# Kernel optimization log

Hardware: AMD Instinct MI355X
Metric: run time of the kernel (lower is better)

The kernel has to match this reference:

```python
import jax, jax.numpy as jnp
import numpy as np

B, S, E, H, FF = 4, 2048, 512, 8, 2048
DH = E // H
EPS = 1e-6


def setup_inputs() -> dict:
    key = jax.random.key(0)
    ks = jax.random.split(key, 16)
    sc = lambda fan_in: 1.0 / np.sqrt(fan_in)
    inp = {
        "x": jax.random.normal(ks[0], (B, S, E), dtype=jnp.float32),
        "src_mask": jnp.ones((B, 1, 1, S), dtype=jnp.int32),
        # attention projections, stored [in, out]
        "wq": jax.random.uniform(ks[1], (E, E), minval=-sc(E), maxval=sc(E)),
        "bq": jnp.zeros((E,), jnp.float32),
        "wk": jax.random.uniform(ks[2], (E, E), minval=-sc(E), maxval=sc(E)),
        "bk": jnp.zeros((E,), jnp.float32),
        "wv": jax.random.uniform(ks[3], (E, E), minval=-sc(E), maxval=sc(E)),
        "bv": jnp.zeros((E,), jnp.float32),
        "wo": jax.random.uniform(ks[4], (E, E), minval=-sc(E), maxval=sc(E)),
        "bo": jnp.zeros((E,), jnp.float32),
        # feed-forward
        "w1": jax.random.uniform(ks[5], (E, FF), minval=-sc(E), maxval=sc(E)),
        "b1": jnp.zeros((FF,), jnp.float32),
        "w2": jax.random.uniform(ks[6], (FF, E), minval=-sc(FF), maxval=sc(FF)),
        "b2": jnp.zeros((E,), jnp.float32),
        # addNormLayer scalar params (alpha init 1, bias init 0)
        "alpha1": jnp.ones((1,), jnp.float32),
        "beta1": jnp.zeros((1,), jnp.float32),
        "alpha2": jnp.ones((1,), jnp.float32),
        "beta2": jnp.zeros((1,), jnp.float32),
    }
    return inp


def _norm(x, alpha, beta):
    # matches torch: mean + unbiased std (ddof=1), eps added to std
    mean = jnp.mean(x, axis=-1, keepdims=True)
    std = jnp.std(x, axis=-1, keepdims=True, ddof=1)
    return alpha * (x - mean) / (std + EPS) + beta


def reference(x, src_mask, wq, bq, wk, bk, wv, bv, wo, bo,
              w1, b1, w2, b2, alpha1, beta1, alpha2, beta2):
    # --- residual 1: pre-norm self-attention ---
    n = _norm(x, alpha1, beta1)  # [B,S,E]
    q = (n @ wq + bq).reshape(B, S, H, DH).transpose(0, 2, 1, 3)  # [B,H,S,DH]
    k = (n @ wk + bk).reshape(B, S, H, DH).transpose(0, 2, 1, 3)
    v = (n @ wv + bv).reshape(B, S, H, DH).transpose(0, 2, 1, 3)
    scores = jnp.einsum('bhqd,bhkd->bhqk', q, k) / np.sqrt(DH)  # [B,H,S,S]
    scores = jnp.where(src_mask == 0, -1e9, scores)
    attn = jax.nn.softmax(scores, axis=-1)
    ctx = jnp.einsum('bhqk,bhkd->bhqd', attn, v)  # [B,H,S,DH]
    ctx = ctx.transpose(0, 2, 1, 3).reshape(B, S, E)
    x = x + (ctx @ wo + bo)
    # --- residual 2: pre-norm FFN ---
    n2 = _norm(x, alpha2, beta2)
    ff = jax.nn.relu(n2 @ w1 + b1) @ w2 + b2
    return x + ff
```

## Files before the change

### kernel.cpp

```cpp
#include <hip/hip_runtime.h>

typedef __bf16 bfrag __attribute__((ext_vector_type(8)));
typedef float f32x4 __attribute__((ext_vector_type(4)));
typedef float f32x16 __attribute__((ext_vector_type(16)));
typedef unsigned short us8 __attribute__((ext_vector_type(8)));
typedef unsigned int u32x2 __attribute__((ext_vector_type(2)));
typedef unsigned int u32x4 __attribute__((ext_vector_type(4)));

__device__ __forceinline__ float bf2f(unsigned short s) {
  unsigned u = ((unsigned)s) << 16;
  float f;
  __builtin_memcpy(&f, &u, 4);
  return f;
}
__device__ __forceinline__ unsigned short f2bf(float f) {
  unsigned u;
  __builtin_memcpy(&u, &f, 4);
  u += 0x7fffu + ((u >> 16) & 1u);
  return (unsigned short)(u >> 16);
}
__device__ __forceinline__ float rdf(const void* p, size_t i, int isf) {
  return isf ? ((const float*)p)[i] : bf2f(((const unsigned short*)p)[i]);
}
__device__ __forceinline__ void gld16(const unsigned short* g, unsigned short* l) {
  __builtin_amdgcn_global_load_lds(
      (const __attribute__((address_space(1))) unsigned int*)g,
      (__attribute__((address_space(3))) unsigned int*)l, 16, 0, 0);
}
__device__ __forceinline__ unsigned cvtpk_bf16(float a, float b) {
  unsigned d;
  asm("v_cvt_pk_bf16_f32 %0, %1, %2" : "=v"(d) : "v"(a), "v"(b));
  return d;
}

template <int XMODE>
__device__ void norm_unit(const void* xin, const void* alpha, const void* beta,
                          unsigned short* out, int isf, int u) {
  constexpr int E = 512;
  int xf = XMODE ? 1 : isf;
  int tid = threadIdx.x;
  int wave = tid >> 6, lane = tid & 63;
  size_t tok = (size_t)u * 4 + wave;
  float v[8];
  if (xf) {
    const float* xp = (const float*)xin + tok * E + lane * 8;
    float4 a0 = *(const float4*)xp;
    float4 a1 = *(const float4*)(xp + 4);
    v[0] = a0.x; v[1] = a0.y; v[2] = a0.z; v[3] = a0.w;
    v[4] = a1.x; v[5] = a1.y; v[6] = a1.z; v[7] = a1.w;
  } else {
    us8 uu = *(const us8*)((const unsigned short*)xin + tok * E + lane * 8);
#pragma unroll
    for (int j = 0; j < 8; j++) v[j] = bf2f(uu[j]);
  }
  float s = 0.f, sq = 0.f;
#pragma unroll
  for (int j = 0; j < 8; j++) { s += v[j]; sq += v[j] * v[j]; }
#pragma unroll
  for (int off = 1; off < 64; off <<= 1) {
    s += __shfl_xor(s, off, 64);
    sq += __shfl_xor(sq, off, 64);
  }
  float mean = s * (1.0f / 512.0f);
  float var = fmaxf((sq - 512.0f * mean * mean) * (1.0f / 511.0f), 0.0f);
  float inv = rdf(alpha, 0, isf) / (sqrtf(var) + 1e-6f);
  float be = rdf(beta, 0, isf);
  us8 ov;
#pragma unroll
  for (int j = 0; j < 8; j++) ov[j] = f2bf((v[j] - mean) * inv + be);
  *(us8*)(out + tok * E + lane * 8) = ov;
}

__global__ __launch_bounds__(256) void setup_k(
    const unsigned short* __restrict__ x16,
    const void* wq, const void* wk, const void* wv, const void* wo,
    const void* w1, const void* w2,
    unsigned short* wqkvT, unsigned short* woT,
    unsigned short* w1T, unsigned short* w2T,
    const void* bq, const void* bk, const void* bv, const void* bo,
    const void* b1, const void* b2, float* __restrict__ bcat,
    const void* alpha1, const void* beta1, unsigned short* __restrict__ n1,
    int* __restrict__ flag) {
  __shared__ unsigned short tile[32][33];
  __shared__ int s_cnt;
  int tid = threadIdx.x;
  int bid = blockIdx.x;
  if (tid == 0) s_cnt = 0;
  __syncthreads();
  {
    int c = 0;
    for (int i = tid; i < 4096; i += 256) {
      unsigned short s = x16[2 * i];
      int e = (s >> 7) & 0xFF;
      if (e > 0xC2 || (e != 0 && e < 0x3D)) c++;
    }
    atomicAdd(&s_cnt, c);
  }
  __syncthreads();
  const int isf = (s_cnt > 256) ? 1 : 0;
  if (bid == 0 && tid == 0) flag[0] = isf;

  if (bid >= 3090) {
    norm_unit<0>(x16, alpha1, beta1, n1, isf, bid - 3090);
    return;
  }
  if (bid >= 3072) {
    int i = (bid - 3072) * 256 + tid;
    if (i < 4608) {
      float v;
      if (i < 512) v = rdf(bq, i, isf);
      else if (i < 1024) v = rdf(bk, i - 512, isf);
      else if (i < 1536) v = rdf(bv, i - 1024, isf);
      else if (i < 2048) v = rdf(bo, i - 1536, isf);
      else if (i < 4096) v = rdf(b1, i - 2048, isf);
      else v = rdf(b2, i - 4096, isf);
      bcat[i] = v;
    }
    return;
  }
  const void* W;
  unsigned short* Wt;
  int K, N, t;
  if (bid < 1024) {
    K = 512; N = 512; t = bid & 255;
    if (bid < 256) { W = wq; Wt = wqkvT; }
    else if (bid < 512) { W = wk; Wt = wqkvT + 262144; }
    else if (bid < 768) { W = wv; Wt = wqkvT + 524288; }
    else { W = wo; Wt = woT; }
  } else if (bid < 2048) {
    W = w1; Wt = w1T; K = 512; N = 2048; t = bid - 1024;
  } else {
    W = w2; Wt = w2T; K = 2048; N = 512; t = bid - 2048;
  }
  int nx = N >> 5;
  int n0 = (t % nx) * 32, k0 = (t / nx) * 32;
#pragma unroll
  for (int i = 0; i < 4; i++) {
    int e = tid + i * 256;
    int r = e >> 5, c = e & 31;
    tile[r][c] = f2bf(rdf(W, (size_t)(k0 + r) * N + n0 + c, isf));
  }
  __syncthreads();
#pragma unroll
  for (int i = 0; i < 4; i++) {
    int e = tid + i * 256;
    int r = e >> 5, c = e & 31;
    Wt[(size_t)(n0 + r) * K + k0 + c] = tile[c][r];
  }
}

__global__ __launch_bounds__(256) void vtrans_k(
    const unsigned short* __restrict__ qkb, unsigned short* __restrict__ vbt) {
  __shared__ unsigned short tile[32][33];
  int tid = threadIdx.x;
  int u = blockIdx.x;
  int s0 = (u & 63) * 32;
  int d0 = ((u >> 6) & 1) * 32;
  int bh = u >> 7, b = bh >> 3, h = bh & 7;
#pragma unroll
  for (int i = 0; i < 4; i++) {
    int e = tid + i * 256;
    int r = e >> 5, c = e & 31;
    tile[r][c] = qkb[((size_t)b * 2048 + s0 + r) * 1536 + 1024 + h * 64 + d0 + c];
  }
  __syncthreads();
#pragma unroll
  for (int i = 0; i < 4; i++) {
    int e = tid + i * 256;
    int r = e >> 5, c = e & 31;
    vbt[((size_t)bh * 64 + d0 + r) * 2048 + s0 + c] = tile[c][r];
  }
}

__global__ __launch_bounds__(256) void norm2_k(
    const void* __restrict__ xin, const void* __restrict__ alpha,
    const void* __restrict__ beta, unsigned short* __restrict__ out,
    const int* __restrict__ flag) {
  norm_unit<1>(xin, alpha, beta, out, flag[0], blockIdx.x);
}

template <int TN, int RES, int OUTM, int RELU>
__global__ __launch_bounds__(256, 3) void gemm2_k(
    const unsigned short* __restrict__ A,
    const unsigned short* __restrict__ Bt,
    const float* __restrict__ bias,
    const void* __restrict__ res,
    void* __restrict__ outp,
    int N, int K, const int* __restrict__ flag) {
  constexpr int MT = (TN == 128) ? 4 : 2;
  constexpr int BROWS = TN / 4;
  __shared__ alignas(16) unsigned short As[128 * 64];
  __shared__ alignas(16) unsigned short Bs[TN * 64];
  int isf = flag[0];
  int outf32 = (OUTM == 1) || (OUTM == 2 && isf);
  int tid = threadIdx.x;
  int wave = tid >> 6, lane = tid & 63;
  int quad = lane >> 4, l16 = lane & 15, l7 = l16 & 7;
  int wm = (TN == 128) ? (wave >> 1) : wave;
  int wn = (TN == 128) ? (wave & 1) : 0;
  size_t m0 = (size_t)blockIdx.x * 128;
  size_t n0 = (size_t)blockIdx.y * TN;

  int lrow = lane >> 3;
  int gcol = 8 * ((lane & 7) ^ lrow);

  const unsigned short* ag = A + (m0 + wave * 32 + lrow) * K + gcol;
  const unsigned short* bg = Bt + (n0 + wave * BROWS + lrow) * K + gcol;
  unsigned short* asl = &As[(wave * 32) * 64];
  unsigned short* bsl = &Bs[(wave * BROWS) * 64];

  f32x4 acc[MT][4];
#pragma unroll
  for (int i = 0; i < MT; i++)
#pragma unroll
    for (int j = 0; j < 4; j++) acc[i][j] = {0.f, 0.f, 0.f, 0.f};

  for (int k0 = 0; k0 < K; k0 += 64) {
    __syncthreads();
#pragma unroll
    for (int c = 0; c < 4; c++)
      gld16(ag + (size_t)(8 * c) * K + k0, asl + (8 * c) * 64);
#pragma unroll
    for (int c = 0; c < BROWS / 8; c++)
      gld16(bg + (size_t)(8 * c) * K + k0, bsl + (8 * c) * 64);
    __syncthreads();
#pragma unroll
    for (int ko = 0; ko < 2; ko++) {
      int slot = ((4 * ko + quad) ^ l7) * 8;
      bfrag af[MT], bf[4];
#pragma unroll
      for (int i = 0; i < MT; i++)
        af[i] = *(const bfrag*)&As[(wm * (MT * 16) + i * 16 + l16) * 64 + slot];
#pragma unroll
      for (int j = 0; j < 4; j++)
        bf[j] = *(const bfrag*)&Bs[(wn * 64 + j * 16 + l16) * 64 + slot];
#pragma unroll
      for (int i = 0; i < MT; i++)
#pragma unroll
        for (int j = 0; j < 4; j++)
          acc[i][j] = __builtin_amdgcn_mfma_f32_16x16x32_bf16(af[i], bf[j], acc[i][j], 0, 0, 0);
    }
  }
#pragma unroll
  for (int j = 0; j < 4; j++) {
    size_t n = n0 + wn * 64 + j * 16 + l16;
    float bv = bias[n];
#pragma unroll
    for (int i = 0; i < MT; i++) {
#pragma unroll
      for (int r = 0; r < 4; r++) {
        size_t m = m0 + wm * (MT * 16) + i * 16 + quad * 4 + r;
        float vv = acc[i][j][r] + bv;
        if (RELU) vv = fmaxf(vv, 0.0f);
        if (RES == 1) vv += rdf(res, m * N + n, isf);
        else if (RES == 2) vv += ((const float*)res)[m * N + n];
        if (outf32) ((float*)outp)[m * N + n] = vv;
        else ((unsigned short*)outp)[m * N + n] = f2bf(vv);
      }
    }
  }
}

__global__ __launch_bounds__(256, 2) void attn_k(
    const unsigned short* __restrict__ qkb,
    const unsigned short* __restrict__ vbt,
    const int* __restrict__ mask,
    unsigned short* __restrict__ ctx) {
  constexpr int S = 2048;
  __shared__ alignas(16) unsigned short Kt[2][2][64 * 64];
  __shared__ alignas(16) unsigned short Vt[2][2][64 * 64];
  __shared__ alignas(16) float mskf[S];
  __shared__ float linv[128];
  int tid = threadIdx.x, wave = tid >> 6, lane = tid & 63;
  int l32 = lane & 31, hi = lane >> 5;

  int lin = blockIdx.x;
  int work = (lin & 7) * 64 + (lin >> 3);
  int bh = work >> 4;
  int q0 = (work & 15) * 128;
  int b = bh >> 3, h = bh & 7;
  size_t rowbase = (size_t)b * S;
  const float SC = 0.18033688f;

  bfrag qf[4];
  {
    const unsigned short* qp =
        qkb + (rowbase + q0 + wave * 32 + l32) * 1536 + h * 64 + hi * 8;
#pragma unroll
    for (int ds = 0; ds < 4; ds++) qf[ds] = *(const bfrag*)(qp + ds * 16);
  }

  int srow_l = lane >> 3;
  int sc = lane & 7;
  int swz = (sc ^ srow_l) * 8;
  const unsigned short* kgb = qkb + 512 + h * 64;
  const unsigned short* vgb = vbt + (size_t)bh * 64 * S;

  const unsigned short* kp[2][2];
  const unsigned short* vp[2][2];
#pragma unroll
  for (int hh = 0; hh < 2; hh++)
#pragma unroll
    for (int i = 0; i < 2; i++) {
      int r = wave * 16 + i * 8 + srow_l;
      kp[hh][i] = kgb + (rowbase + hh * 64 + r) * 1536 + swz;
      vp[hh][i] = vgb + (size_t)r * S + hh * 64 + swz;
    }

  auto STAGE = [&](int buf) {
#pragma unroll
    for (int hh = 0; hh < 2; hh++)
#pragma unroll
      for (int i = 0; i < 2; i++) {
        gld16(kp[hh][i], &Kt[buf][hh][(wave * 16 + i * 8) * 64]);
        kp[hh][i] += 128 * 1536;
        gld16(vp[hh][i], &Vt[buf][hh][(wave * 16 + i * 8) * 64]);
        vp[hh][i] += 128;
      }
  };

  f32x16 o[2];
#pragma unroll
  for (int i = 0; i < 16; i++) { o[0][i] = 0.f; o[1][i] = 0.f; }
  float l_i = 0.f;

  auto QK = [&](int hh, int cur, f32x16* pacc) {
#pragma unroll
    for (int t = 0; t < 2; t++) {
#pragma unroll
      for (int i = 0; i < 16; i++) pacc[t][i] = 0.f;
      int r = t * 32 + l32;
#pragma unroll
      for (int ds = 0; ds < 4; ds++) {
        int phys = ((2 * ds + hi) ^ (l32 & 7)) * 8;
        bfrag kf = *(const bfrag*)&Kt[cur][hh][r * 64 + phys];
        pacc[t] = __builtin_amdgcn_mfma_f32_32x32x16_bf16(kf, qf[ds], pacc[t], 0, 0, 0);
      }
    }
  };
  auto SM = [&](int hh, int kt, const f32x16* pacc, unsigned* pb) {
#pragma unroll
    for (int t = 0; t < 2; t++) {
#pragma unroll
      for (int g = 0; g < 4; g++) {
        float4 m4 = *(const float4*)&mskf[kt + hh * 64 + t * 32 + g * 8 + hi * 4];
        float p0 = __builtin_amdgcn_exp2f(fmaf(pacc[t][g * 4 + 0], SC, m4.x));
        float p1 = __builtin_amdgcn_exp2f(fmaf(pacc[t][g * 4 + 1], SC, m4.y));
        float p2 = __builtin_amdgcn_exp2f(fmaf(pacc[t][g * 4 + 2], SC, m4.z));
        float p3 = __builtin_amdgcn_exp2f(fmaf(pacc[t][g * 4 + 3], SC, m4.w));
        l_i += (p0 + p1) + (p2 + p3);
        pb[t * 8 + g * 2] = cvtpk_bf16(p0, p1);
        pb[t * 8 + g * 2 + 1] = cvtpk_bf16(p2, p3);
      }
    }
  };
  auto PV = [&](int hh, int cur, const unsigned* pb) {
#pragma unroll
    for (int ks = 0; ks < 4; ks++) {
      int t = ks >> 1, e = ks & 1;
      u32x2 sA = __builtin_amdgcn_permlane32_swap(pb[t * 8 + 4 * e + 0], pb[t * 8 + 4 * e + 2], false, false);
      u32x2 sB = __builtin_amdgcn_permlane32_swap(pb[t * 8 + 4 * e + 1], pb[t * 8 + 4 * e + 3], false, false);
      u32x4 pw = {sA.x, sB.x, sA.y, sB.y};
      bfrag pf = __builtin_bit_cast(bfrag, pw);
#pragma unroll
      for (int dt = 0; dt < 2; dt++) {
        int r = dt * 32 + l32;
        int phys = ((2 * ks + hi) ^ (l32 & 7)) * 8;
        bfrag vf = *(const bfrag*)&Vt[cur][hh][r * 64 + phys];
        o[dt] = __builtin_amdgcn_mfma_f32_32x32x16_bf16(pf, vf, o[dt], 0, 0, 0);
      }
    }
  };

  STAGE(0);
  for (int i = tid; i < S; i += 256) mskf[i] = mask[rowbase + i] ? 0.0f : -1e5f;
  __syncthreads();

  for (int it = 0; it < S / 128; it++) {
    int kt = it * 128;
    int cur = it & 1;
    if (it + 1 < S / 128) STAGE(cur ^ 1);

    f32x16 pacc0[2], pacc1[2];
    unsigned pb0[16], pb1[16];
    __builtin_amdgcn_s_setprio(1);
    QK(0, cur, pacc0);
    __builtin_amdgcn_s_setprio(0);
    SM(0, kt, pacc0, pb0);
    __builtin_amdgcn_s_setprio(1);
    QK(1, cur, pacc1);
    PV(0, cur, pb0);
    __builtin_amdgcn_s_setprio(0);
    SM(1, kt, pacc1, pb1);
    __builtin_amdgcn_s_setprio(1);
    PV(1, cur, pb1);
    __builtin_amdgcn_s_setprio(0);
    __syncthreads();
  }

  {
    unsigned lu = __builtin_bit_cast(unsigned, l_i);
    u32x2 lr = __builtin_amdgcn_permlane32_swap(lu, lu, false, false);
    float l_tot = __builtin_bit_cast(float, lr.x) + __builtin_bit_cast(float, lr.y);
    if (lane < 32) linv[wave * 32 + l32] = 1.0f / fmaxf(l_tot, 1e-30f);
  }
  __syncthreads();
#pragma unroll
  for (int dt = 0; dt < 2; dt++) {
#pragma unroll
    for (int reg = 0; reg < 16; reg++) {
      int ql = (reg & 3) + 8 * (reg >> 2) + 4 * hi;
      size_t qrow = rowbase + q0 + wave * 32 + ql;
      ctx[qrow * 512 + h * 64 + dt * 32 + l32] =
          f2bf(o[dt][reg] * linv[wave * 32 + ql]);
    }
  }
}

extern "C" void kernel_launch(void* const* d_in, const int* in_sizes, int n_in,
                              void* d_out, int out_size, void* d_ws, size_t ws_size,
                              hipStream_t stream) {
  const unsigned short* x = (const unsigned short*)d_in[0];
  const int* mask         = (const int*)d_in[1];
  const void* wq = d_in[2];  const void* bq = d_in[3];
  const void* wk = d_in[4];  const void* bk = d_in[5];
  const void* wv = d_in[6];  const void* bv = d_in[7];
  const void* wo = d_in[8];  const void* bo = d_in[9];
  const void* w1 = d_in[10]; const void* b1 = d_in[11];
  const void* w2 = d_in[12]; const void* b2 = d_in[13];
  const void* alpha1 = d_in[14]; const void* beta1 = d_in[15];
  const void* alpha2 = d_in[16]; const void* beta2 = d_in[17];

  char* ws = (char*)d_ws;
  int* flag            = (int*)(ws + 0);
  unsigned short* wqkvT= (unsigned short*)(ws + 65536);
  unsigned short* woT  = (unsigned short*)(ws + 1638400);
  unsigned short* w1T  = (unsigned short*)(ws + 2162688);
  unsigned short* w2T  = (unsigned short*)(ws + 4259840);
  float*          bcat = (float*)         (ws + 6356992);
  float*          x1   = (float*)         (ws + 6422528);
  unsigned short* n1   = (unsigned short*)(ws + 23199744);
  unsigned short* qkb  = (unsigned short*)(ws + 31588352);
  unsigned short* vbt  = (unsigned short*)(ws + 56754176);
  unsigned short* ff1  = qkb;

  dim3 blk(256);

  setup_k<<<5138, blk, 0, stream>>>(x, wq, wk, wv, wo, w1, w2,
                                    wqkvT, woT, w1T, w2T,
                                    bq, bk, bv, bo, b1, b2, bcat,
                                    alpha1, beta1, n1, flag);
  gemm2_k<128, 0, 0, 0><<<dim3(64, 12), blk, 0, stream>>>(n1, wqkvT, bcat, nullptr, qkb, 1536, 512, flag);
  vtrans_k<<<4096, blk, 0, stream>>>(qkb, vbt);
  attn_k<<<512, blk, 0, stream>>>(qkb, vbt, mask, n1);
  gemm2_k<64, 1, 1, 0><<<dim3(64, 8), blk, 0, stream>>>(n1, woT, bcat + 1536, (const void*)x, x1, 512, 512, flag);
  norm2_k<<<2048, blk, 0, stream>>>(x1, alpha2, beta2, n1, flag);
  gemm2_k<128, 0, 0, 1><<<dim3(64, 16), blk, 0, stream>>>(n1, w1T, bcat + 2048, nullptr, ff1, 2048, 512, flag);
  gemm2_k<64, 2, 2, 0><<<dim3(64, 8), blk, 0, stream>>>(ff1, w2T, bcat + 4096, x1, d_out, 512, 2048, flag);
}
```

Measured before the change: 276.6 us.

## Add all-ones mask fast path and interleave attention MFMA with exp via sched barriers

The attention kernel now checks at runtime whether the whole mask row is nonzero. If it is, it runs a templated loop body that skips the per-element mask loads and fmaf adds. The loop is also reordered so both QK halves are issued first, and sched_group_barrier hints interleave MFMA, LDS reads and VALU work. The setprio calls are removed and the accumulator zeroing is folded into the first MFMA. The mask check is a genuine runtime branch, so masked inputs stay correct, but it adds an atomic and an extra barrier plus longer register lifetimes.

```diff
diff --git a/kernel.cpp b/kernel.cpp
--- a/kernel.cpp
+++ b/kernel.cpp
@@ -1,4 +1,5 @@
 #include <hip/hip_runtime.h>
+#include <type_traits>
 
 typedef __bf16 bfrag __attribute__((ext_vector_type(8)));
 typedef float f32x4 __attribute__((ext_vector_type(4)));
@@ -271,6 +272,7 @@
   __shared__ alignas(16) unsigned short Vt[2][2][64 * 64];
   __shared__ alignas(16) float mskf[S];
   __shared__ float linv[128];
+  __shared__ int s_all;
   int tid = threadIdx.x, wave = tid >> 6, lane = tid & 63;
   int l32 = lane & 31, hi = lane >> 5;
 
@@ -322,81 +324,109 @@
   f32x16 o[2];
 #pragma unroll
   for (int i = 0; i < 16; i++) { o[0][i] = 0.f; o[1][i] = 0.f; }
+  f32x16 z16;
+#pragma unroll
+  for (int i = 0; i < 16; i++) z16[i] = 0.f;
   float l_i = 0.f;
 
-  auto QK = [&](int hh, int cur, f32x16* pacc) {
-#pragma unroll
-    for (int t = 0; t < 2; t++) {
-#pragma unroll
-      for (int i = 0; i < 16; i++) pacc[t][i] = 0.f;
-      int r = t * 32 + l32;
-#pragma unroll
-      for (int ds = 0; ds < 4; ds++) {
-        int phys = ((2 * ds + hi) ^ (l32 & 7)) * 8;
-        bfrag kf = *(const bfrag*)&Kt[cur][hh][r * 64 + phys];
-        pacc[t] = __builtin_amdgcn_mfma_f32_32x32x16_bf16(kf, qf[ds], pacc[t], 0, 0, 0);
+  STAGE(0);
+  if (tid == 0) s_all = 1;
+  __syncthreads();
+  {
+    int ok = 1;
+    for (int i = tid; i < S; i += 256) {
+      int mv = mask[rowbase + i];
+      ok &= (mv != 0);
+      mskf[i] = mv ? 0.0f : -1e5f;
+    }
+    atomicAnd(&s_all, ok);
+  }
+  __syncthreads();
+  int am = s_all;
+
+  auto BODY = [&](auto amc) {
+    constexpr bool AM = decltype(amc)::value;
+    for (int it = 0; it < S / 128; it++) {
+      int kt = it * 128;
+      int cur = it & 1;
+      if (it + 1 < S / 128) STAGE(cur ^ 1);
+
+      f32x16 pacc0[2], pacc1[2];
+      unsigned pb0[16], pb1[16];
+
+#pragma unroll
+      for (int hh = 0; hh < 2; hh++) {
+        f32x16* pa = hh ? pacc1 : pacc0;
+#pragma unroll
+        for (int t = 0; t < 2; t++) {
+          int r = t * 32 + l32;
+#pragma unroll
+          for (int ds = 0; ds < 4; ds++) {
+            int phys = ((2 * ds + hi) ^ (l32 & 7)) * 8;
+            bfrag kf = *(const bfrag*)&Kt[cur][hh][r * 64 + phys];
+            pa[t] = __builtin_amdgcn_mfma_f32_32x32x16_bf16(
+                kf, qf[ds], ds == 0 ? z16 : pa[t], 0, 0, 0);
+          }
+        }
       }
+
+#pragma unroll
+      for (int hh = 0; hh < 2; hh++) {
+        const f32x16* pacc = hh ? pacc1 : pacc0;
+        unsigned* pb = hh ? pb1 : pb0;
+#pragma unroll
+        for (int t = 0; t < 2; t++) {
+#pragma unroll
+          for (int g = 0; g < 4; g++) {
+            float p0, p1, p2, p3;
+            if constexpr (AM) {
+              p0 = __builtin_amdgcn_exp2f(pacc[t][g * 4 + 0] * SC);
+              p1 = __builtin_amdgcn_exp2f(pacc[t][g * 4 + 1] * SC);
+              p2 = __builtin_amdgcn_exp2f(pacc[t][g * 4 + 2] * SC);
+              p3 = __builtin_amdgcn_exp2f(pacc[t][g * 4 + 3] * SC);
+            } else {
+              float4 m4 = *(const float4*)&mskf[kt + hh * 64 + t * 32 + g * 8 + hi * 4];
+              p0 = __builtin_amdgcn_exp2f(fmaf(pacc[t][g * 4 + 0], SC, m4.x));
+              p1 = __builtin_amdgcn_exp2f(fmaf(pacc[t][g * 4 + 1], SC, m4.y));
+              p2 = __builtin_amdgcn_exp2f(fmaf(pacc[t][g * 4 + 2], SC, m4.z));
+              p3 = __builtin_amdgcn_exp2f(fmaf(pacc[t][g * 4 + 3], SC, m4.w));
+            }
+            l_i += (p0 + p1) + (p2 + p3);
+            pb[t * 8 + g * 2] = cvtpk_bf16(p0, p1);
+            pb[t * 8 + g * 2 + 1] = cvtpk_bf16(p2, p3);
+          }
+        }
+#pragma unroll
+        for (int ks = 0; ks < 4; ks++) {
+          int t = ks >> 1, e = ks & 1;
+          u32x2 sA = __builtin_amdgcn_permlane32_swap(
+              pb[t * 8 + 4 * e + 0], pb[t * 8 + 4 * e + 2], false, false);
+          u32x2 sB = __builtin_amdgcn_permlane32_swap(
+              pb[t * 8 + 4 * e + 1], pb[t * 8 + 4 * e + 3], false, false);
+          u32x4 pw = {sA.x, sB.x, sA.y, sB.y};
+          bfrag pf = __builtin_bit_cast(bfrag, pw);
+#pragma unroll
+          for (int dt = 0; dt < 2; dt++) {
+            int r = dt * 32 + l32;
+            int phys = ((2 * ks + hi) ^ (l32 & 7)) * 8;
+            bfrag vf = *(const bfrag*)&Vt[cur][hh][r * 64 + phys];
+            o[dt] = __builtin_amdgcn_mfma_f32_32x32x16_bf16(pf, vf, o[dt], 0, 0, 0);
+          }
+        }
+      }
+
+      __builtin_amdgcn_sched_group_barrier(0x020, 8, 0);
+#pragma unroll
+      for (int z = 0; z < 16; z++) {
+        __builtin_amdgcn_sched_group_barrier(0x100, 2, 0);
+        __builtin_amdgcn_sched_group_barrier(0x008, 2, 0);
+        __builtin_amdgcn_sched_group_barrier(0x002, 16, 0);
+      }
+      __syncthreads();
     }
   };
-  auto SM = [&](int hh, int kt, const f32x16* pacc, unsigned* pb) {
-#pragma unroll
-    for (int t = 0; t < 2; t++) {
-#pragma unroll
-      for (int g = 0; g < 4; g++) {
-        float4 m4 = *(const float4*)&mskf[kt + hh * 64 + t * 32 + g * 8 + hi * 4];
-        float p0 = __builtin_amdgcn_exp2f(fmaf(pacc[t][g * 4 + 0], SC, m4.x));
-        float p1 = __builtin_amdgcn_exp2f(fmaf(pacc[t][g * 4 + 1], SC, m4.y));
-        float p2 = __builtin_amdgcn_exp2f(fmaf(pacc[t][g * 4 + 2], SC, m4.z));
-        float p3 = __builtin_amdgcn_exp2f(fmaf(pacc[t][g * 4 + 3], SC, m4.w));
-        l_i += (p0 + p1) + (p2 + p3);
-        pb[t * 8 + g * 2] = cvtpk_bf16(p0, p1);
-        pb[t * 8 + g * 2 + 1] = cvtpk_bf16(p2, p3);
-      }
-    }
-  };
-  auto PV = [&](int hh, int cur, const unsigned* pb) {
-#pragma unroll
-    for (int ks = 0; ks < 4; ks++) {
-      int t = ks >> 1, e = ks & 1;
-      u32x2 sA = __builtin_amdgcn_permlane32_swap(pb[t * 8 + 4 * e + 0], pb[t * 8 + 4 * e + 2], false, false);
-      u32x2 sB = __builtin_amdgcn_permlane32_swap(pb[t * 8 + 4 * e + 1], pb[t * 8 + 4 * e + 3], false, false);
-      u32x4 pw = {sA.x, sB.x, sA.y, sB.y};
-      bfrag pf = __builtin_bit_cast(bfrag, pw);
-#pragma unroll
-      for (int dt = 0; dt < 2; dt++) {
-        int r = dt * 32 + l32;
-        int phys = ((2 * ks + hi) ^ (l32 & 7)) * 8;
-        bfrag vf = *(const bfrag*)&Vt[cur][hh][r * 64 + phys];
-        o[dt] = __builtin_amdgcn_mfma_f32_32x32x16_bf16(pf, vf, o[dt], 0, 0, 0);
-      }
-    }
-  };
-
-  STAGE(0);
-  for (int i = tid; i < S; i += 256) mskf[i] = mask[rowbase + i] ? 0.0f : -1e5f;
-  __syncthreads();
-
-  for (int it = 0; it < S / 128; it++) {
-    int kt = it * 128;
-    int cur = it & 1;
-    if (it + 1 < S / 128) STAGE(cur ^ 1);
-
-    f32x16 pacc0[2], pacc1[2];
-    unsigned pb0[16], pb1[16];
-    __builtin_amdgcn_s_setprio(1);
-    QK(0, cur, pacc0);
-    __builtin_amdgcn_s_setprio(0);
-    SM(0, kt, pacc0, pb0);
-    __builtin_amdgcn_s_setprio(1);
-    QK(1, cur, pacc1);
-    PV(0, cur, pb0);
-    __builtin_amdgcn_s_setprio(0);
-    SM(1, kt, pacc1, pb1);
-    __builtin_amdgcn_s_setprio(1);
-    PV(1, cur, pb1);
-    __builtin_amdgcn_s_setprio(0);
-    __syncthreads();
-  }
+  if (am) BODY(std::integral_constant<bool, true>{});
+  else    BODY(std::integral_constant<bool, false>{});
 
   {
     unsigned lu = __builtin_bit_cast(unsigned, l_i);
```

Result: no change. 272.5 us (-1.5%).
